# Kernel optimization log

Measured on AMD Instinct MI355X. Metric: run time of the kernel, lower is better.

The kernel has to match this reference:

```python
import jax, jax.numpy as jnp
import numpy as np

EXPAND = 1

def setup_inputs() -> dict:
    key = jax.random.key(0)
    k1, k2 = jax.random.split(key)
    B = 2097152
    pre = jax.random.normal(k1, (B, 25), dtype=jnp.float32)
    tar = jax.random.normal(k2, (B, 25), dtype=jnp.float32)
    return {"pre": pre, "tar": tar}

def reference(pre, tar):
    B = pre.shape[0]
    # 6 independent 4-way softmaxes per sample, scaled by 3*expand
    logits = pre[:, :24].reshape(B, 6, 4)
    out = (3.0 * EXPAND) * jax.nn.softmax(logits, axis=-1)  # [B, 6, 4]
    # out[24] = relu(pre[:,24]) in the original, but loss only uses out[0:24],
    # so the relu does not affect the returned loss.
    diff = out.reshape(B, 24) - tar[:, :24]
    # per-sample mean over 24 elems, then mean over batch
    per_sample = jnp.mean(diff * diff, axis=-1)  # [B]
    return jnp.mean(per_sample)
```

## Files before the change

kernel.cpp:

```cpp
#include <hip/hip_runtime.h>


constexpr int B_ROWS   = 2097152;
constexpr int ROWW     = 25;
constexpr int TILE_ROWS = 256;
constexpr int NTHREADS = 256;
constexpr int NBLOCKS  = 2048;
constexpr int NTILES   = B_ROWS / TILE_ROWS;
constexpr int TILE_F4  = TILE_ROWS * ROWW / 4;

__global__ __launch_bounds__(NTHREADS)
void soft_add_partial(const float* __restrict__ pre,
                      const float* __restrict__ tar,
                      float* __restrict__ partial)
{
    __shared__ float s_pre[TILE_ROWS * ROWW];
    __shared__ float s_tar[TILE_ROWS * ROWW];
    __shared__ float s_red[NTHREADS / 64];

    const int tid = threadIdx.x;
    float acc = 0.0f;

    for (int tile = blockIdx.x; tile < NTILES; tile += gridDim.x) {
        const long base = (long)tile * TILE_ROWS * ROWW;
        const float4* gp = reinterpret_cast<const float4*>(pre + base);
        const float4* gt = reinterpret_cast<const float4*>(tar + base);
        float4* sp = reinterpret_cast<float4*>(s_pre);
        float4* st = reinterpret_cast<float4*>(s_tar);

        for (int i = tid; i < TILE_F4; i += NTHREADS) {
            sp[i] = gp[i];
            st[i] = gt[i];
        }
        __syncthreads();

        const float* rp = s_pre + tid * ROWW;
        const float* rt = s_tar + tid * ROWW;
        #pragma unroll
        for (int g = 0; g < 6; ++g) {
            const float v0 = rp[4*g + 0];
            const float v1 = rp[4*g + 1];
            const float v2 = rp[4*g + 2];
            const float v3 = rp[4*g + 3];
            const float m  = fmaxf(fmaxf(v0, v1), fmaxf(v2, v3));
            const float e0 = __expf(v0 - m);
            const float e1 = __expf(v1 - m);
            const float e2 = __expf(v2 - m);
            const float e3 = __expf(v3 - m);
            const float r  = 3.0f / (e0 + e1 + e2 + e3);
            const float d0 = e0 * r - rt[4*g + 0];
            const float d1 = e1 * r - rt[4*g + 1];
            const float d2 = e2 * r - rt[4*g + 2];
            const float d3 = e3 * r - rt[4*g + 3];
            acc += d0 * d0;
            acc += d1 * d1;
            acc += d2 * d2;
            acc += d3 * d3;
        }
        __syncthreads();
    }

    #pragma unroll
    for (int off = 32; off > 0; off >>= 1)
        acc += __shfl_down(acc, off, 64);
    const int wave = tid >> 6;
    const int lane = tid & 63;
    if (lane == 0) s_red[wave] = acc;
    __syncthreads();
    if (tid == 0) {
        float s = 0.0f;
        #pragma unroll
        for (int w = 0; w < NTHREADS / 64; ++w) s += s_red[w];
        partial[blockIdx.x] = s;
    }
}

__global__ __launch_bounds__(NTHREADS)
void soft_add_final(const float* __restrict__ partial, float* __restrict__ out)
{
    __shared__ float s_red[NTHREADS / 64];
    const int tid = threadIdx.x;
    float acc = 0.0f;
    for (int i = tid; i < NBLOCKS; i += NTHREADS)
        acc += partial[i];
    #pragma unroll
    for (int off = 32; off > 0; off >>= 1)
        acc += __shfl_down(acc, off, 64);
    const int wave = tid >> 6;
    const int lane = tid & 63;
    if (lane == 0) s_red[wave] = acc;
    __syncthreads();
    if (tid == 0) {
        float s = 0.0f;
        #pragma unroll
        for (int w = 0; w < NTHREADS / 64; ++w) s += s_red[w];
        out[0] = s * (1.0f / (24.0f * (float)B_ROWS));
    }
}

extern "C" void kernel_launch(void* const* d_in, const int* in_sizes, int n_in,
                              void* d_out, int out_size, void* d_ws, size_t ws_size,
                              hipStream_t stream)
{
    const float* pre = (const float*)d_in[0];
    const float* tar = (const float*)d_in[1];
    float* out = (float*)d_out;
    float* partial = (float*)d_ws;

    soft_add_partial<<<NBLOCKS, NTHREADS, 0, stream>>>(pre, tar, partial);
    soft_add_final<<<1, NTHREADS, 0, stream>>>(partial, out);
}
```

Baseline: 84.40 us.

## Keep target tile in registers and write softmax back to shared memory

Instead of staging both pre and tar in LDS, tar is loaded straight into per-thread float4 registers in the coalesced global layout. Each thread computes the softmax of its row in place in shared memory, and after a barrier the squared differences are taken element-wise against the register copy, with a column counter masking out column 24. This halves LDS use per block, which could allow more resident blocks, and removes the strided LDS reads of tar. It adds an extra barrier per tile, a modulo and column bookkeeping per element, and more registers.

```diff
diff --git a/kernel.cpp b/kernel.cpp
--- a/kernel.cpp
+++ b/kernel.cpp
@@ -1,13 +1,14 @@
 #include <hip/hip_runtime.h>
 
 
-constexpr int B_ROWS   = 2097152;
-constexpr int ROWW     = 25;
+constexpr int B_ROWS    = 2097152;
+constexpr int ROWW      = 25;
 constexpr int TILE_ROWS = 256;
-constexpr int NTHREADS = 256;
-constexpr int NBLOCKS  = 2048;
-constexpr int NTILES   = B_ROWS / TILE_ROWS;
-constexpr int TILE_F4  = TILE_ROWS * ROWW / 4;
+constexpr int NTHREADS  = 256;
+constexpr int NBLOCKS   = 2048;
+constexpr int NTILES    = B_ROWS / TILE_ROWS;
+constexpr int TILE_F4   = TILE_ROWS * ROWW / 4;
+constexpr int F4_PER_T  = (TILE_F4 + NTHREADS - 1) / NTHREADS;
 
 __global__ __launch_bounds__(NTHREADS)
 void soft_add_partial(const float* __restrict__ pre,
@@ -15,7 +16,6 @@
                       float* __restrict__ partial)
 {
     __shared__ float s_pre[TILE_ROWS * ROWW];
-    __shared__ float s_tar[TILE_ROWS * ROWW];
     __shared__ float s_red[NTHREADS / 64];
 
     const int tid = threadIdx.x;
@@ -26,16 +26,21 @@
         const float4* gp = reinterpret_cast<const float4*>(pre + base);
         const float4* gt = reinterpret_cast<const float4*>(tar + base);
         float4* sp = reinterpret_cast<float4*>(s_pre);
-        float4* st = reinterpret_cast<float4*>(s_tar);
 
-        for (int i = tid; i < TILE_F4; i += NTHREADS) {
-            sp[i] = gp[i];
-            st[i] = gt[i];
+        float4 rt[F4_PER_T];
+        #pragma unroll
+        for (int j = 0; j < F4_PER_T; ++j) {
+            const int i = tid + j * NTHREADS;
+            if (i < TILE_F4) rt[j] = gt[i];
+        }
+        #pragma unroll
+        for (int j = 0; j < F4_PER_T; ++j) {
+            const int i = tid + j * NTHREADS;
+            if (i < TILE_F4) sp[i] = gp[i];
         }
         __syncthreads();
 
-        const float* rp = s_pre + tid * ROWW;
-        const float* rt = s_tar + tid * ROWW;
+        float* rp = s_pre + tid * ROWW;
         #pragma unroll
         for (int g = 0; g < 6; ++g) {
             const float v0 = rp[4*g + 0];
@@ -48,14 +53,26 @@
             const float e2 = __expf(v2 - m);
             const float e3 = __expf(v3 - m);
             const float r  = 3.0f / (e0 + e1 + e2 + e3);
-            const float d0 = e0 * r - rt[4*g + 0];
-            const float d1 = e1 * r - rt[4*g + 1];
-            const float d2 = e2 * r - rt[4*g + 2];
-            const float d3 = e3 * r - rt[4*g + 3];
-            acc += d0 * d0;
-            acc += d1 * d1;
-            acc += d2 * d2;
-            acc += d3 * d3;
+            rp[4*g + 0] = e0 * r;
+            rp[4*g + 1] = e1 * r;
+            rp[4*g + 2] = e2 * r;
+            rp[4*g + 3] = e3 * r;
+        }
+        __syncthreads();
+
+        #pragma unroll
+        for (int j = 0; j < F4_PER_T; ++j) {
+            const int i = tid + j * NTHREADS;
+            if (i < TILE_F4) {
+                const float4 o = sp[i];
+                const float4 t = rt[j];
+                int col = (4 * i) % 25;
+                float d;
+                d = o.x - t.x; if (col != 24) acc += d * d; col = (col == 24) ? 0 : col + 1;
+                d = o.y - t.y; if (col != 24) acc += d * d; col = (col == 24) ? 0 : col + 1;
+                d = o.z - t.z; if (col != 24) acc += d * d; col = (col == 24) ? 0 : col + 1;
+                d = o.w - t.w; if (col != 24) acc += d * d;
+            }
         }
         __syncthreads();
     }
```

Result: no change. 83.79 us (-0.7%).

## Per-wave double-buffered direct global-to-LDS loads with register-held targets

Applied to the files above, without the earlier changes.

Replaces the block-wide shared-memory tile loop with per-wave 64-row tiles fetched into LDS through global_load_lds DMA, double-buffered with explicit vmcnt waits, so the loads for the next tile overlap compute on the current one. Target values go straight into registers as coalesced float4 loads, and block-level __syncthreads barriers are removed. Softmax outputs are written back to LDS and reread in the flat layout to match the targets, masking column 24. This adds hand-written waitcnt sequencing and hardcodes exactly four tiles per wave, which ties the kernel to this problem size and grid.

```diff
diff --git a/kernel.cpp b/kernel.cpp
--- a/kernel.cpp
+++ b/kernel.cpp
@@ -3,74 +3,152 @@
 
 constexpr int B_ROWS   = 2097152;
 constexpr int ROWW     = 25;
-constexpr int TILE_ROWS = 256;
+constexpr int WTILE    = 64;
+constexpr int WT_FLOAT = WTILE * ROWW;
 constexpr int NTHREADS = 256;
+constexpr int WAVES_PB = NTHREADS / 64;
 constexpr int NBLOCKS  = 2048;
-constexpr int NTILES   = B_ROWS / TILE_ROWS;
-constexpr int TILE_F4  = TILE_ROWS * ROWW / 4;
+constexpr int NWAVES   = NBLOCKS * WAVES_PB;
+constexpr int NWTILES  = B_ROWS / WTILE;
+constexpr int NITER    = NWTILES / NWAVES;
+
+#define DMA_TILE(GSRC, LBUF) do {                                              \
+    _Pragma("unroll")                                                          \
+    for (int c = 0; c < 6; ++c) {                                              \
+        const float* g_ = (GSRC) + c * 256 + lane * 4;                         \
+        __builtin_amdgcn_global_load_lds(                                      \
+            (const __attribute__((address_space(1))) void*)g_,                 \
+            (__attribute__((address_space(3))) void*)((LBUF) + c * 256),       \
+            16, 0, 0);                                                         \
+    }                                                                          \
+    const float* gt_ = (GSRC) + 1536 + lane;                                   \
+    __builtin_amdgcn_global_load_lds(                                          \
+        (const __attribute__((address_space(1))) void*)gt_,                    \
+        (__attribute__((address_space(3))) void*)((LBUF) + 1536),              \
+        4, 0, 0);                                                              \
+} while (0)
+
+#define LOAD_TAR(RT, GBASE) do {                                               \
+    const float4* gt4_ = reinterpret_cast<const float4*>(GBASE);               \
+    _Pragma("unroll")                                                          \
+    for (int j = 0; j < 7; ++j) {                                              \
+        const int i_ = lane + j * 64;                                          \
+        if (j < 6 || lane < 16) (RT)[j] = gt4_[i_];                            \
+    }                                                                          \
+} while (0)
+
+#define COMPUTE_TILE(BUF, RT) do {                                             \
+    const float* rowp_ = (BUF) + lane * ROWW;                                  \
+    float o_[24];                                                              \
+    _Pragma("unroll")                                                          \
+    for (int g6 = 0; g6 < 6; ++g6) {                                           \
+        const float v0 = rowp_[4*g6 + 0];                                      \
+        const float v1 = rowp_[4*g6 + 1];                                      \
+        const float v2 = rowp_[4*g6 + 2];                                      \
+        const float v3 = rowp_[4*g6 + 3];                                      \
+        const float m_ = fmaxf(fmaxf(v0, v1), fmaxf(v2, v3));                  \
+        const float e0 = __expf(v0 - m_);                                      \
+        const float e1 = __expf(v1 - m_);                                      \
+        const float e2 = __expf(v2 - m_);                                      \
+        const float e3 = __expf(v3 - m_);                                      \
+        const float r_ = 3.0f / (e0 + e1 + e2 + e3);                           \
+        o_[4*g6 + 0] = e0 * r_;                                                \
+        o_[4*g6 + 1] = e1 * r_;                                                \
+        o_[4*g6 + 2] = e2 * r_;                                                \
+        o_[4*g6 + 3] = e3 * r_;                                                \
+    }                                                                          \
+    float* roww_ = (BUF) + lane * ROWW;                                        \
+    _Pragma("unroll")                                                          \
+    for (int m2 = 0; m2 < 24; ++m2) roww_[m2] = o_[m2];                        \
+    asm volatile("s_waitcnt lgkmcnt(0)" ::: "memory");                         \
+    __builtin_amdgcn_sched_barrier(0);                                         \
+    const float4* bf4_ = reinterpret_cast<const float4*>(BUF);                 \
+    _Pragma("unroll")                                                          \
+    for (int j = 0; j < 7; ++j) {                                              \
+        const int i_ = lane + j * 64;                                          \
+        if (j < 6 || lane < 16) {                                              \
+            const float4 ov = bf4_[i_];                                        \
+            const float4 tv = (RT)[j];                                         \
+            int col_ = (4 * i_) % 25;                                          \
+            float d_;                                                          \
+            d_ = ov.x - tv.x; if (col_ != 24) acc += d_ * d_;                  \
+            col_ = (col_ == 24) ? 0 : col_ + 1;                                \
+            d_ = ov.y - tv.y; if (col_ != 24) acc += d_ * d_;                  \
+            col_ = (col_ == 24) ? 0 : col_ + 1;                                \
+            d_ = ov.z - tv.z; if (col_ != 24) acc += d_ * d_;                  \
+            col_ = (col_ == 24) ? 0 : col_ + 1;                                \
+            d_ = ov.w - tv.w; if (col_ != 24) acc += d_ * d_;                  \
+        }                                                                      \
+    }                                                                          \
+} while (0)
+
+#define WAIT_VM14() do {                                                       \
+    asm volatile("s_waitcnt vmcnt(14)" ::: "memory");                          \
+    __builtin_amdgcn_sched_barrier(0);                                         \
+} while (0)
+#define WAIT_VM0() do {                                                        \
+    asm volatile("s_waitcnt vmcnt(0)" ::: "memory");                           \
+    __builtin_amdgcn_sched_barrier(0);                                         \
+} while (0)
 
 __global__ __launch_bounds__(NTHREADS)
 void soft_add_partial(const float* __restrict__ pre,
                       const float* __restrict__ tar,
                       float* __restrict__ partial)
 {
-    __shared__ float s_pre[TILE_ROWS * ROWW];
-    __shared__ float s_tar[TILE_ROWS * ROWW];
-    __shared__ float s_red[NTHREADS / 64];
+    __shared__ float lds[WAVES_PB][2][WT_FLOAT];
+    __shared__ float s_red[WAVES_PB];
 
-    const int tid = threadIdx.x;
+    const int tid  = threadIdx.x;
+    const int lane = tid & 63;
+    const int wv   = tid >> 6;
+    const int gw   = blockIdx.x * WAVES_PB + wv;
+
+    float* buf0 = &lds[wv][0][0];
+    float* buf1 = &lds[wv][1][0];
+
+    const float* p0 = pre + (long)(gw + 0 * NWAVES) * WT_FLOAT;
+    const float* p1 = pre + (long)(gw + 1 * NWAVES) * WT_FLOAT;
+    const float* p2 = pre + (long)(gw + 2 * NWAVES) * WT_FLOAT;
+    const float* p3 = pre + (long)(gw + 3 * NWAVES) * WT_FLOAT;
+    const float* t0 = tar + (long)(gw + 0 * NWAVES) * WT_FLOAT;
+    const float* t1 = tar + (long)(gw + 1 * NWAVES) * WT_FLOAT;
+    const float* t2 = tar + (long)(gw + 2 * NWAVES) * WT_FLOAT;
+    const float* t3 = tar + (long)(gw + 3 * NWAVES) * WT_FLOAT;
+
     float acc = 0.0f;
+    float4 rtA[7], rtB[7];
 
-    for (int tile = blockIdx.x; tile < NTILES; tile += gridDim.x) {
-        const long base = (long)tile * TILE_ROWS * ROWW;
-        const float4* gp = reinterpret_cast<const float4*>(pre + base);
-        const float4* gt = reinterpret_cast<const float4*>(tar + base);
-        float4* sp = reinterpret_cast<float4*>(s_pre);
-        float4* st = reinterpret_cast<float4*>(s_tar);
+    DMA_TILE(p0, buf0);
+    LOAD_TAR(rtA, t0);
 
-        for (int i = tid; i < TILE_F4; i += NTHREADS) {
-            sp[i] = gp[i];
-            st[i] = gt[i];
-        }
-        __syncthreads();
+    DMA_TILE(p1, buf1);
+    LOAD_TAR(rtB, t1);
+    WAIT_VM14();
+    COMPUTE_TILE(buf0, rtA);
 
-        const float* rp = s_pre + tid * ROWW;
-        const float* rt = s_tar + tid * ROWW;
-        #pragma unroll
-        for (int g = 0; g < 6; ++g) {
-            const float v0 = rp[4*g + 0];
-            const float v1 = rp[4*g + 1];
-            const float v2 = rp[4*g + 2];
-            const float v3 = rp[4*g + 3];
-            const float m  = fmaxf(fmaxf(v0, v1), fmaxf(v2, v3));
-            const float e0 = __expf(v0 - m);
-            const float e1 = __expf(v1 - m);
-            const float e2 = __expf(v2 - m);
-            const float e3 = __expf(v3 - m);
-            const float r  = 3.0f / (e0 + e1 + e2 + e3);
-            const float d0 = e0 * r - rt[4*g + 0];
-            const float d1 = e1 * r - rt[4*g + 1];
-            const float d2 = e2 * r - rt[4*g + 2];
-            const float d3 = e3 * r - rt[4*g + 3];
-            acc += d0 * d0;
-            acc += d1 * d1;
-            acc += d2 * d2;
-            acc += d3 * d3;
-        }
-        __syncthreads();
-    }
+    DMA_TILE(p2, buf0);
+    LOAD_TAR(rtA, t2);
+    WAIT_VM14();
+    COMPUTE_TILE(buf1, rtB);
+
+    DMA_TILE(p3, buf1);
+    LOAD_TAR(rtB, t3);
+    WAIT_VM14();
+    COMPUTE_TILE(buf0, rtA);
+
+    WAIT_VM0();
+    COMPUTE_TILE(buf1, rtB);
 
     #pragma unroll
     for (int off = 32; off > 0; off >>= 1)
         acc += __shfl_down(acc, off, 64);
-    const int wave = tid >> 6;
-    const int lane = tid & 63;
-    if (lane == 0) s_red[wave] = acc;
+    if (lane == 0) s_red[wv] = acc;
     __syncthreads();
     if (tid == 0) {
         float s = 0.0f;
         #pragma unroll
-        for (int w = 0; w < NTHREADS / 64; ++w) s += s_red[w];
+        for (int w = 0; w < WAVES_PB; ++w) s += s_red[w];
         partial[blockIdx.x] = s;
     }
 }
```

New measurement: 80.87 us, median of 2. 4.2% less time.
